# Performance work log

Measured on AMD Instinct MI355X. Metric: run time of the kernel, lower is better.

Reference implementation:

```python
import jax, jax.numpy as jnp
import numpy as np

EMBED = 2048
HEADS = 16
DFF = 4 * EMBED
EPS = 1e-5


def layernorm(x, g, b):
    mu = jnp.mean(x, axis=-1, keepdims=True)
    var = jnp.var(x, axis=-1, keepdims=True)
    return (x - mu) * jax.lax.rsqrt(var + EPS) * g + b


def setup_inputs() -> dict:
    key = jax.random.key(0)
    ks = jax.random.split(key, 16)
    s = 1.0 / np.sqrt(EMBED)
    sf = 1.0 / np.sqrt(DFF)
    return {
        "x": jax.random.normal(ks[0], (2, 2048, EMBED), jnp.float32),
        "Wq": jax.random.normal(ks[1], (EMBED, EMBED), jnp.float32) * s,
        "bq": jnp.zeros((EMBED,), jnp.float32),
        "Wk": jax.random.normal(ks[2], (EMBED, EMBED), jnp.float32) * s,
        "bk": jnp.zeros((EMBED,), jnp.float32),
        "Wv": jax.random.normal(ks[3], (EMBED, EMBED), jnp.float32) * s,
        "bv": jnp.zeros((EMBED,), jnp.float32),
        "Wo": jax.random.normal(ks[4], (EMBED, EMBED), jnp.float32) * s,
        "bo": jnp.zeros((EMBED,), jnp.float32),
        "g1": jnp.ones((EMBED,), jnp.float32),
        "b1": jnp.zeros((EMBED,), jnp.float32),
        "g2": jnp.ones((EMBED,), jnp.float32),
        "b2": jnp.zeros((EMBED,), jnp.float32),
        "W1": jax.random.normal(ks[5], (EMBED, DFF), jnp.float32) * s,
        "bf1": jnp.zeros((DFF,), jnp.float32),
        "W2": jax.random.normal(ks[6], (DFF, EMBED), jnp.float32) * sf,
        "bf2": jnp.zeros((EMBED,), jnp.float32),
    }


def reference(x, Wq, bq, Wk, bk, Wv, bv, Wo, bo, g1, b1, g2, b2, W1, bf1, W2, bf2):
    B, N, C = x.shape
    H = HEADS
    hd = C // H
    # QKV projections -> [B, H, N, hd]
    def split_heads(t):
        return t.reshape(B, N, H, hd).transpose(0, 2, 1, 3)
    q = split_heads(x @ Wq + bq)
    k = split_heads(x @ Wk + bk)
    v = split_heads(x @ Wv + bv)
    # scores [B, H, N, N]
    attn = jnp.einsum('bhqd,bhkd->bhqk', q, k) / np.sqrt(hd)
    attn = jax.nn.softmax(attn, axis=-1)
    out = jnp.einsum('bhqk,bhkd->bhqd', attn, v)
    out = out.transpose(0, 2, 1, 3).reshape(B, N, C)
    out = out @ Wo + bo
    h = layernorm(x + out, g1, b1)
    ff = jax.nn.gelu(h @ W1 + bf1, approximate=False) @ W2 + bf2
    return layernorm(h + ff, g2, b2)
```

## Files before the change

kernel.cpp:

```cpp
#include <hip/hip_runtime.h>
#include <math.h>

#define EMBED 2048
#define DFF   8192
#define TOK   4096
#define SEQ   2048
#define HEADS 16
#define HD    128
#define LDQ   6144

typedef __attribute__((ext_vector_type(8))) short short8;
typedef __attribute__((ext_vector_type(4))) float f32x4;

__device__ __forceinline__ unsigned short f2bf(float f) {
    unsigned int u = __float_as_uint(f);
    return (unsigned short)((u + 0x7FFFu + ((u >> 16) & 1u)) >> 16);
}
__device__ __forceinline__ float bf2f(unsigned short s) {
    return __uint_as_float(((unsigned int)s) << 16);
}

__device__ __forceinline__ void async16(const void* g, void* l) {
    __builtin_amdgcn_global_load_lds((const __attribute__((address_space(1))) void*)g,
                                     (__attribute__((address_space(3))) void*)l, 16, 0, 0);
}

__device__ __forceinline__ float gelu_fast(float v) {
    const float y = 1.5957691216057308f * (v + 0.044715f * v * v * v);
    return v / (1.0f + __expf(-y));
}

template<int MODE>
__global__ __launch_bounds__(256, 2)
void gemm_bf16(const unsigned short* __restrict__ A, const unsigned short* __restrict__ B,
               const float* __restrict__ bias, const void* __restrict__ resid,
               unsigned short* __restrict__ C, int M, int N, int K, int lda)
{
    __shared__ __align__(16) float smemf[8448];
    unsigned short* As = (unsigned short*)smemf;
    unsigned short* Bs = As + 8192;
    float* Cs = smemf;

    const int t = threadIdx.x;
    const int w = t >> 6, l = t & 63;
    const int quad = l >> 4, m16 = l & 15;
    const long bm = (long)blockIdx.y * 128, bn = (long)blockIdx.x * 128;
    const int wr = (w >> 1)*64, wc = (w & 1)*64;

    f32x4 acc[4][4] = {};

    const int srow = w*16 + (l >> 2);
    const int sslot = l & 3;
    const unsigned short* Ag = A + (size_t)bm*lda;
    const unsigned short* Bg = B + (size_t)bn*K;

#pragma unroll
    for (int u = 0; u < 2; ++u) {
        const int row = u*64 + srow;
        const int c = sslot ^ ((row >> 1) & 3);
        async16(Ag + (size_t)row*lda + c*8, &As[u*2048 + w*512]);
        async16(Bg + (size_t)row*K   + c*8, &Bs[u*2048 + w*512]);
    }

    const int iters = K >> 5;
    for (int it = 0; it < iters; ++it) {
        __syncthreads();
        if (it + 1 < iters) {
            const int k0 = (it + 1) << 5;
            const int bo = ((it + 1) & 1) * 4096;
#pragma unroll
            for (int u = 0; u < 2; ++u) {
                const int row = u*64 + srow;
                const int c = sslot ^ ((row >> 1) & 3);
                async16(Ag + (size_t)row*lda + k0 + c*8, &As[bo + u*2048 + w*512]);
                async16(Bg + (size_t)row*K   + k0 + c*8, &Bs[bo + u*2048 + w*512]);
            }
        }
        const int co = (it & 1) * 4096;
        short8 af[4], bf[4];
#pragma unroll
        for (int s = 0; s < 4; ++s) {
            const int ra = wr + s*16 + m16;
            const int sla = quad ^ ((ra >> 1) & 3);
            af[s] = *(const short8*)&As[co + ra*32 + sla*8];
            const int rb = wc + s*16 + m16;
            const int slb = quad ^ ((rb >> 1) & 3);
            bf[s] = *(const short8*)&Bs[co + rb*32 + slb*8];
        }
#pragma unroll
        for (int ms = 0; ms < 4; ++ms)
#pragma unroll
            for (int ns = 0; ns < 4; ++ns)
                acc[ms][ns] = __builtin_amdgcn_mfma_f32_16x16x32_bf16(af[ms], bf[ns], acc[ms][ns], 0, 0, 0);
    }

    const int ecol = (t & 15) * 8;
    float bias8[8];
#pragma unroll
    for (int i = 0; i < 8; ++i) bias8[i] = bias[bn + ecol + i];

#pragma unroll
    for (int pass = 0; pass < 2; ++pass) {
        __syncthreads();
        if ((w >> 1) == pass) {
#pragma unroll
            for (int ms = 0; ms < 4; ++ms)
#pragma unroll
                for (int ns = 0; ns < 4; ++ns)
#pragma unroll
                    for (int r = 0; r < 4; ++r)
                        Cs[(ms*16 + quad*4 + r)*132 + wc + ns*16 + m16] = acc[ms][ns][r];
        }
        __syncthreads();
#pragma unroll
        for (int j = 0; j < 4; ++j) {
            const int row = j*16 + (t >> 4);
            float v[8];
            *(f32x4*)&v[0] = *(const f32x4*)&Cs[row*132 + ecol];
            *(f32x4*)&v[4] = *(const f32x4*)&Cs[row*132 + ecol + 4];
            const long gr = bm + pass*64 + row;
            const long go = gr*N + bn + ecol;
            float r8[8];
            if (MODE == 1) {
                *(f32x4*)&r8[0] = *(const f32x4*)((const float*)resid + go);
                *(f32x4*)&r8[4] = *(const f32x4*)((const float*)resid + go + 4);
            }
            short8 rb16;
            if (MODE == 3) rb16 = *(const short8*)((const unsigned short*)resid + go);
            short8 o;
#pragma unroll
            for (int i = 0; i < 8; ++i) {
                float y = v[i] + bias8[i];
                if (MODE == 1) y += r8[i];
                if (MODE == 3) y += bf2f((unsigned short)rb16[i]);
                if (MODE == 2) y = gelu_fast(y);
                o[i] = (short)f2bf(y);
            }
            *(short8*)&C[go] = o;
        }
    }
}

__global__ __launch_bounds__(256, 2)
void attn_flash(unsigned short* __restrict__ qkv)
{
    __shared__ unsigned short Ks2[2][64*128];
    __shared__ unsigned short Vt[128*72];
    __shared__ unsigned short Ps[4*16*72];

    const int t = threadIdx.x;
    const int w = t >> 6, l = t & 63;
    const int quad = l >> 4, m16 = l & 15;

    const int qt = blockIdx.x & 31;
    const int bh = blockIdx.x >> 5;
    const int b = bh >> 4, h = bh & 15;

    const long rowq = (long)b*SEQ + qt*64;
    const long rowb = (long)b*SEQ;
    const int qc = h*HD;
    const int kc = EMBED + h*HD;
    const int vc = 2*EMBED + h*HD;

    const int rbase = w*4 + (l >> 4);
    const int slot  = l & 15;
    const int vslot = t & 15;
    const int vrp   = t >> 4;

    unsigned short* Qs = Ks2[1];

    short8 va[2], vb[2];
#pragma unroll
    for (int u = 0; u < 2; ++u) {
        const int rp = u*16 + vrp;
        va[u] = *(const short8*)(qkv + (rowb + 2*rp    )*LDQ + vc + vslot*8);
        vb[u] = *(const short8*)(qkv + (rowb + 2*rp + 1)*LDQ + vc + vslot*8);
    }
#pragma unroll
    for (int u = 0; u < 4; ++u) {
        const int row = u*16 + rbase;
        const int c = slot ^ ((row >> 1) & 7);
        async16(qkv + (rowq + row)*LDQ + qc + c*8, Qs + u*2048 + w*512);
        async16(qkv + (rowb + row)*LDQ + kc + c*8, &Ks2[0][u*2048 + w*512]);
    }
#pragma unroll
    for (int u = 0; u < 2; ++u) {
        const int rp = u*16 + vrp;
#pragma unroll
        for (int i = 0; i < 8; ++i) {
            const int d = vslot*8 + i;
            const int col = (2*rp) ^ (((d >> 5) & 3) << 3);
            unsigned int pv = (unsigned int)(unsigned short)va[u][i] |
                              ((unsigned int)(unsigned short)vb[u][i] << 16);
            *(unsigned int*)&Vt[d*72 + col] = pv;
        }
    }
    __syncthreads();

    short8 af[4];
#pragma unroll
    for (int ks = 0; ks < 4; ++ks) {
        const int row = w*16 + m16;
        const int sl = (4*ks + quad) ^ ((row >> 1) & 7);
        af[ks] = *(const short8*)&Qs[row*128 + sl*8];
    }
    __syncthreads();

    f32x4 O[8] = {};
    float mrun[4] = {-1e30f,-1e30f,-1e30f,-1e30f};
    float lrun[4] = {0.f,0.f,0.f,0.f};
    unsigned short* Pw = Ps + w*16*72;

    for (int kt = 0; kt < SEQ/64; ++kt) {
        const int cur = kt & 1;
        const bool pre = (kt + 1 < SEQ/64);
        const long rowkv = rowb + (long)(kt + 1)*64;

        if (pre) {
#pragma unroll
            for (int u = 0; u < 2; ++u) {
                const int rp = u*16 + vrp;
                va[u] = *(const short8*)(qkv + (rowkv + 2*rp    )*LDQ + vc + vslot*8);
                vb[u] = *(const short8*)(qkv + (rowkv + 2*rp + 1)*LDQ + vc + vslot*8);
            }
#pragma unroll
            for (int u = 0; u < 4; ++u) {
                const int row = u*16 + rbase;
                const int c = slot ^ ((row >> 1) & 7);
                async16(qkv + (rowkv + row)*LDQ + kc + c*8, &Ks2[cur^1][u*2048 + w*512]);
            }
        }

        f32x4 S[4];
#pragma unroll
        for (int ns = 0; ns < 4; ++ns) {
            f32x4 a = {0.f,0.f,0.f,0.f};
            const int row = ns*16 + m16;
            const int swr = (row >> 1) & 7;
#pragma unroll
            for (int ks = 0; ks < 4; ++ks) {
                const int sl = (4*ks + quad) ^ swr;
                const short8 bfr = *(const short8*)&Ks2[cur][row*128 + sl*8];
                a = __builtin_amdgcn_mfma_f32_16x16x32_bf16(af[ks], bfr, a, 0, 0, 0);
            }
#pragma unroll
            for (int r = 0; r < 4; ++r) a[r] *= 0.08838834764831845f;
            S[ns] = a;
        }

        float al[4], rs[4];
#pragma unroll
        for (int r = 0; r < 4; ++r) {
            float tm = fmaxf(fmaxf(S[0][r], S[1][r]), fmaxf(S[2][r], S[3][r]));
            tm = fmaxf(tm, __shfl_xor(tm, 1));
            tm = fmaxf(tm, __shfl_xor(tm, 2));
            tm = fmaxf(tm, __shfl_xor(tm, 4));
            tm = fmaxf(tm, __shfl_xor(tm, 8));
            const float mn = fmaxf(mrun[r], tm);
            al[r] = __expf(mrun[r] - mn);
            mrun[r] = mn;
            rs[r] = 0.f;
        }
#pragma unroll
        for (int ns = 0; ns < 4; ++ns)
#pragma unroll
            for (int r = 0; r < 4; ++r) {
                const float p = __expf(S[ns][r] - mrun[r]);
                rs[r] += p;
                Pw[(quad*4 + r)*72 + ns*16 + m16] = f2bf(p);
            }
#pragma unroll
        for (int r = 0; r < 4; ++r) {
            rs[r] += __shfl_xor(rs[r], 1);
            rs[r] += __shfl_xor(rs[r], 2);
            rs[r] += __shfl_xor(rs[r], 4);
            rs[r] += __shfl_xor(rs[r], 8);
            lrun[r] = lrun[r]*al[r] + rs[r];
        }
        if (__any((al[0] != 1.f) | (al[1] != 1.f) | (al[2] != 1.f) | (al[3] != 1.f))) {
#pragma unroll
            for (int i = 0; i < 8; ++i)
#pragma unroll
                for (int r = 0; r < 4; ++r) O[i][r] *= al[r];
        }

#pragma unroll
        for (int ks2 = 0; ks2 < 2; ++ks2) {
            const short8 ap = *(const short8*)&Pw[m16*72 + ks2*32 + quad*8];
#pragma unroll
            for (int ds = 0; ds < 8; ++ds) {
                const int d = ds*16 + m16;
                const int jcol = (ks2*32 + quad*8) ^ (((d >> 5) & 3) << 3);
                const short8 bv = *(const short8*)&Vt[d*72 + jcol];
                O[ds] = __builtin_amdgcn_mfma_f32_16x16x32_bf16(ap, bv, O[ds], 0, 0, 0);
            }
        }

        __syncthreads();
        if (pre) {
#pragma unroll
            for (int u = 0; u < 2; ++u) {
                const int rp = u*16 + vrp;
#pragma unroll
                for (int i = 0; i < 8; ++i) {
                    const int d = vslot*8 + i;
                    const int col = (2*rp) ^ (((d >> 5) & 3) << 3);
                    unsigned int pv = (unsigned int)(unsigned short)va[u][i] |
                                      ((unsigned int)(unsigned short)vb[u][i] << 16);
                    *(unsigned int*)&Vt[d*72 + col] = pv;
                }
            }
        }
        __syncthreads();
    }

    float inv[4];
#pragma unroll
    for (int r = 0; r < 4; ++r) inv[r] = 1.0f / lrun[r];
#pragma unroll
    for (int ds = 0; ds < 8; ++ds)
#pragma unroll
        for (int r = 0; r < 4; ++r) {
            const long row = rowq + w*16 + quad*4 + r;
            qkv[row*LDQ + qc + ds*16 + m16] = f2bf(O[ds][r] * inv[r]);
        }
}

template<int OUTF32>
__global__ __launch_bounds__(256)
void ln_bf16(const unsigned short* __restrict__ X, const float* __restrict__ g,
             const float* __restrict__ be, void* __restrict__ Y)
{
    __shared__ float r1[256], r2[256];
    const int t = threadIdx.x;
    const long row = blockIdx.x;
    const unsigned short* x = X + row*EMBED;
    float v[8];
    const short8 xv = *(const short8*)(x + t*8);
    float s = 0.f, s2 = 0.f;
#pragma unroll
    for (int i = 0; i < 8; ++i) {
        v[i] = bf2f((unsigned short)xv[i]);
        s += v[i]; s2 += v[i]*v[i];
    }
    r1[t] = s; r2[t] = s2;
    __syncthreads();
    for (int k = 128; k > 0; k >>= 1) {
        if (t < k) { r1[t] += r1[t+k]; r2[t] += r2[t+k]; }
        __syncthreads();
    }
    const float mu = r1[0] * (1.0f/EMBED);
    const float var = r2[0] * (1.0f/EMBED) - mu*mu;
    const float rstd = rsqrtf(var + 1e-5f);
    if (OUTF32) {
        float* y = (float*)Y + row*EMBED + t*8;
#pragma unroll
        for (int i = 0; i < 8; ++i) y[i] = (v[i]-mu)*rstd*g[t*8+i] + be[t*8+i];
    } else {
        unsigned short* y = (unsigned short*)Y + row*EMBED;
        short8 o;
#pragma unroll
        for (int i = 0; i < 8; ++i) o[i] = (short)f2bf((v[i]-mu)*rstd*g[t*8+i] + be[t*8+i]);
        *(short8*)(y + t*8) = o;
    }
}

__global__ __launch_bounds__(256)
void cvt_transpose(const float* __restrict__ W, unsigned short* __restrict__ Wt, int K, int N)
{
    __shared__ unsigned short T[32][33];
    const int t = threadIdx.x;
    const long n0 = (long)blockIdx.x*32, k0 = (long)blockIdx.y*32;
    {
        const int r = t >> 3, c = (t & 7)*4;
        const float4 vv = *(const float4*)&W[(k0 + r)*N + n0 + c];
        T[r][c+0] = f2bf(vv.x); T[r][c+1] = f2bf(vv.y);
        T[r][c+2] = f2bf(vv.z); T[r][c+3] = f2bf(vv.w);
    }
    __syncthreads();
    const int rn = t >> 3, kk = (t & 7)*4;
    unsigned int p0 = (unsigned int)T[kk+0][rn] | ((unsigned int)T[kk+1][rn] << 16);
    unsigned int p1 = (unsigned int)T[kk+2][rn] | ((unsigned int)T[kk+3][rn] << 16);
    unsigned int* dst = (unsigned int*)&Wt[(n0 + rn)*K + k0 + kk];
    dst[0] = p0; dst[1] = p1;
}

__global__ __launch_bounds__(256)
void cvt_f32_bf16(const float* __restrict__ X, unsigned short* __restrict__ Y, long n)
{
    const long i = ((long)blockIdx.x*256 + threadIdx.x)*8;
    if (i >= n) return;
    const float4 a = *(const float4*)&X[i];
    const float4 b = *(const float4*)&X[i+4];
    short8 o;
    o[0]=(short)f2bf(a.x); o[1]=(short)f2bf(a.y); o[2]=(short)f2bf(a.z); o[3]=(short)f2bf(a.w);
    o[4]=(short)f2bf(b.x); o[5]=(short)f2bf(b.y); o[6]=(short)f2bf(b.z); o[7]=(short)f2bf(b.w);
    *(short8*)&Y[i] = o;
}

__global__ __launch_bounds__(256)
void concat_bias(const float* __restrict__ bq, const float* __restrict__ bk,
                 const float* __restrict__ bv, float* __restrict__ out)
{
    const int i = blockIdx.x*256 + threadIdx.x;
    if (i < 2048) out[i] = bq[i];
    else if (i < 4096) out[i] = bk[i-2048];
    else if (i < 6144) out[i] = bv[i-4096];
}

extern "C" void kernel_launch(void* const* d_in, const int* in_sizes, int n_in,
                              void* d_out, int out_size, void* d_ws, size_t ws_size,
                              hipStream_t stream)
{
    const float* x   = (const float*)d_in[0];
    const float* Wq  = (const float*)d_in[1];
    const float* bq  = (const float*)d_in[2];
    const float* Wk  = (const float*)d_in[3];
    const float* bk  = (const float*)d_in[4];
    const float* Wv  = (const float*)d_in[5];
    const float* bv  = (const float*)d_in[6];
    const float* Wo  = (const float*)d_in[7];
    const float* bo  = (const float*)d_in[8];
    const float* g1  = (const float*)d_in[9];
    const float* b1  = (const float*)d_in[10];
    const float* g2v = (const float*)d_in[11];
    const float* b2v = (const float*)d_in[12];
    const float* W1  = (const float*)d_in[13];
    const float* bf1 = (const float*)d_in[14];
    const float* W2  = (const float*)d_in[15];
    const float* bf2 = (const float*)d_in[16];
    float* out = (float*)d_out;

    char* ws = (char*)d_ws;
    unsigned short* Wqkvt = (unsigned short*)(ws + 0);
    unsigned short* Wot   = (unsigned short*)(ws + 25165824);
    unsigned short* W1t   = (unsigned short*)(ws + 33554432);
    unsigned short* W2t   = (unsigned short*)(ws + 67108864);
    float*          bqkv  = (float*)         (ws + 100663296);
    char* arenaA = ws + 100687872;
    unsigned short* xb   = (unsigned short*)(arenaA);
    unsigned short* qkv  = (unsigned short*)(arenaA + 16777216);
    unsigned short* res1 = (unsigned short*)(arenaA);
    unsigned short* ff   = (unsigned short*)(arenaA);
    unsigned short* hb   = (unsigned short*)(ws + 167796736);
    unsigned short* res2 = (unsigned short*)(ws + 0);

    const dim3 blk(256);

    cvt_transpose<<<dim3(64,64),  blk, 0, stream>>>(Wq, Wqkvt,             2048, 2048);
    cvt_transpose<<<dim3(64,64),  blk, 0, stream>>>(Wk, Wqkvt + 2048*2048, 2048, 2048);
    cvt_transpose<<<dim3(64,64),  blk, 0, stream>>>(Wv, Wqkvt + 2*2048*2048, 2048, 2048);
    cvt_transpose<<<dim3(64,64),  blk, 0, stream>>>(Wo, Wot, 2048, 2048);
    cvt_transpose<<<dim3(256,64), blk, 0, stream>>>(W1, W1t, 2048, 8192);
    cvt_transpose<<<dim3(64,256), blk, 0, stream>>>(W2, W2t, 8192, 2048);
    concat_bias<<<dim3(24), blk, 0, stream>>>(bq, bk, bv, bqkv);
    cvt_f32_bf16<<<dim3(4096), blk, 0, stream>>>(x, xb, (long)TOK*EMBED);

    gemm_bf16<0><<<dim3(48,32), blk, 0, stream>>>(xb, Wqkvt, bqkv, nullptr, qkv, TOK, 6144, 2048, 2048);
    attn_flash<<<dim3(1024), blk, 0, stream>>>(qkv);
    gemm_bf16<1><<<dim3(16,32), blk, 0, stream>>>(qkv, Wot, bo, x, res1, TOK, 2048, 2048, 6144);
    ln_bf16<0><<<dim3(4096), blk, 0, stream>>>(res1, g1, b1, hb);
    gemm_bf16<2><<<dim3(64,32), blk, 0, stream>>>(hb, W1t, bf1, nullptr, ff, TOK, 8192, 2048, 2048);
    gemm_bf16<3><<<dim3(16,32), blk, 0, stream>>>(ff, W2t, bf2, hb, res2, TOK, 2048, 8192, 8192);
    ln_bf16<1><<<dim3(4096), blk, 0, stream>>>(res2, g2v, b2v, out);
}
```

Measured before the change: 968.7 us.

## Double-buffer V tile, drop a barrier, use exp2 softmax, remap attention blocks

The V tile in the flash-attention kernel is now double-buffered. The transposed write of the next tile happens before the PV MFMAs on the current tile, which removes one __syncthreads per KV iteration. Softmax folds log2(e) into the score scale and calls the hardware exp2 directly instead of __expf. The block index is remapped so that consecutive blocks cover different batch-heads, which changes L2 locality. The extra buffer adds about 18KB of LDS per block and could reduce occupancy.

```diff
diff --git a/kernel.cpp b/kernel.cpp
--- a/kernel.cpp
+++ b/kernel.cpp
@@ -18,6 +18,9 @@
 }
 __device__ __forceinline__ float bf2f(unsigned short s) {
     return __uint_as_float(((unsigned int)s) << 16);
+}
+__device__ __forceinline__ float exp2_fast(float x) {
+    return __builtin_amdgcn_exp2f(x);
 }
 
 __device__ __forceinline__ void async16(const void* g, void* l) {
@@ -145,15 +148,16 @@
 void attn_flash(unsigned short* __restrict__ qkv)
 {
     __shared__ unsigned short Ks2[2][64*128];
-    __shared__ unsigned short Vt[128*72];
+    __shared__ unsigned short Vt2[2][128*72];
     __shared__ unsigned short Ps[4*16*72];
 
     const int t = threadIdx.x;
     const int w = t >> 6, l = t & 63;
     const int quad = l >> 4, m16 = l & 15;
 
-    const int qt = blockIdx.x & 31;
-    const int bh = blockIdx.x >> 5;
+    const int dd = blockIdx.x;
+    const int bh = (dd & 7)*4 + ((dd >> 3) >> 5);
+    const int qt = (dd >> 3) & 31;
     const int b = bh >> 4, h = bh & 15;
 
     const long rowq = (long)b*SEQ + qt*64;
@@ -188,11 +192,11 @@
         const int rp = u*16 + vrp;
 #pragma unroll
         for (int i = 0; i < 8; ++i) {
-            const int d = vslot*8 + i;
-            const int col = (2*rp) ^ (((d >> 5) & 3) << 3);
+            const int dv = vslot*8 + i;
+            const int col = (2*rp) ^ (((dv >> 5) & 3) << 3);
             unsigned int pv = (unsigned int)(unsigned short)va[u][i] |
                               ((unsigned int)(unsigned short)vb[u][i] << 16);
-            *(unsigned int*)&Vt[d*72 + col] = pv;
+            *(unsigned int*)&Vt2[0][dv*72 + col] = pv;
         }
     }
     __syncthreads();
@@ -210,6 +214,7 @@
     float mrun[4] = {-1e30f,-1e30f,-1e30f,-1e30f};
     float lrun[4] = {0.f,0.f,0.f,0.f};
     unsigned short* Pw = Ps + w*16*72;
+    const float SC = 0.08838834764831845f * 1.4426950408889634f;
 
     for (int kt = 0; kt < SEQ/64; ++kt) {
         const int cur = kt & 1;
@@ -244,7 +249,7 @@
                 a = __builtin_amdgcn_mfma_f32_16x16x32_bf16(af[ks], bfr, a, 0, 0, 0);
             }
 #pragma unroll
-            for (int r = 0; r < 4; ++r) a[r] *= 0.08838834764831845f;
+            for (int r = 0; r < 4; ++r) a[r] *= SC;
             S[ns] = a;
         }
 
@@ -257,7 +262,7 @@
             tm = fmaxf(tm, __shfl_xor(tm, 4));
             tm = fmaxf(tm, __shfl_xor(tm, 8));
             const float mn = fmaxf(mrun[r], tm);
-            al[r] = __expf(mrun[r] - mn);
+            al[r] = exp2_fast(mrun[r] - mn);
             mrun[r] = mn;
             rs[r] = 0.f;
         }
@@ -265,7 +270,7 @@
         for (int ns = 0; ns < 4; ++ns)
 #pragma unroll
             for (int r = 0; r < 4; ++r) {
-                const float p = __expf(S[ns][r] - mrun[r]);
+                const float p = exp2_fast(S[ns][r] - mrun[r]);
                 rs[r] += p;
                 Pw[(quad*4 + r)*72 + ns*16 + m16] = f2bf(p);
             }
@@ -284,33 +289,33 @@
                 for (int r = 0; r < 4; ++r) O[i][r] *= al[r];
         }
 
+        if (pre) {
+#pragma unroll
+            for (int u = 0; u < 2; ++u) {
+                const int rp = u*16 + vrp;
+#pragma unroll
+                for (int i = 0; i < 8; ++i) {
+                    const int dv = vslot*8 + i;
+                    const int col = (2*rp) ^ (((dv >> 5) & 3) << 3);
+                    unsigned int pv = (unsigned int)(unsigned short)va[u][i] |
+                                      ((unsigned int)(unsigned short)vb[u][i] << 16);
+                    *(unsigned int*)&Vt2[cur^1][dv*72 + col] = pv;
+                }
+            }
+        }
+
 #pragma unroll
         for (int ks2 = 0; ks2 < 2; ++ks2) {
             const short8 ap = *(const short8*)&Pw[m16*72 + ks2*32 + quad*8];
 #pragma unroll
             for (int ds = 0; ds < 8; ++ds) {
-                const int d = ds*16 + m16;
-                const int jcol = (ks2*32 + quad*8) ^ (((d >> 5) & 3) << 3);
-                const short8 bv = *(const short8*)&Vt[d*72 + jcol];
+                const int dv = ds*16 + m16;
+                const int jcol = (ks2*32 + quad*8) ^ (((dv >> 5) & 3) << 3);
+                const short8 bv = *(const short8*)&Vt2[cur][dv*72 + jcol];
                 O[ds] = __builtin_amdgcn_mfma_f32_16x16x32_bf16(ap, bv, O[ds], 0, 0, 0);
             }
         }
 
-        __syncthreads();
-        if (pre) {
-#pragma unroll
-            for (int u = 0; u < 2; ++u) {
-                const int rp = u*16 + vrp;
-#pragma unroll
-                for (int i = 0; i < 8; ++i) {
-                    const int d = vslot*8 + i;
-                    const int col = (2*rp) ^ (((d >> 5) & 3) << 3);
-                    unsigned int pv = (unsigned int)(unsigned short)va[u][i] |
-                                      ((unsigned int)(unsigned short)vb[u][i] << 16);
-                    *(unsigned int*)&Vt[d*72 + col] = pv;
-                }
-            }
-        }
         __syncthreads();
     }
 
```

New measurement: 956.0 us. About the same (-1.3%).
